# Optimization experiments

Hardware: AMD Instinct MI355X
Metric: run time of the kernel (lower is better)

## Reference

```python
import jax, jax.numpy as jnp
import numpy as np
import math

B, N, D, H, FFN = 64, 128, 128, 4, 128
NEG = -9e15
LRELU_SLOPE = 0.2  # LeakyReLU alpha from init_kwargs


def entmax_bisect(x, alpha, n_iter=30):
    # alpha-entmax via bisection (entmax package algorithm); alpha broadcastable, in (1, 2].
    am1 = alpha - 1.0
    x = x * am1
    d = x.shape[-1]
    max_val = jnp.max(x, axis=-1, keepdims=True)
    tau_lo = max_val - 1.0
    tau_hi = max_val - (1.0 / d) ** am1

    def p(tau):
        return jnp.maximum(x - tau, 0.0) ** (1.0 / am1)

    f_lo = jnp.sum(p(tau_lo), axis=-1, keepdims=True) - 1.0
    for _ in range(n_iter):  # fixed iteration count -> jit friendly
        tau_m = 0.5 * (tau_lo + tau_hi)
        f_m = jnp.sum(p(tau_m), axis=-1, keepdims=True) - 1.0
        same = (f_m * f_lo) >= 0
        tau_lo = jnp.where(same, tau_m, tau_lo)
        f_lo = jnp.where(same, f_m, f_lo)
        tau_hi = jnp.where(same, tau_hi, tau_m)
    pm = p(0.5 * (tau_lo + tau_hi))
    return pm / jnp.sum(pm, axis=-1, keepdims=True)


def layernorm(x, g, b, eps=1e-5):
    mu = jnp.mean(x, axis=-1, keepdims=True)
    var = jnp.var(x, axis=-1, keepdims=True)
    return (x - mu) / jnp.sqrt(var + eps) * g + b


def setup_inputs() -> dict:
    key = jax.random.key(0)
    ks = jax.random.split(key, 24)
    s = 0.05
    sw = 1.0 / math.sqrt(D)
    return {
        "hidden": jax.random.normal(ks[0], (B, N, D), jnp.float32),
        "adj": jax.random.randint(ks[1], (B, N, N), 0, 5, jnp.int32),
        "a0": jax.random.normal(ks[2], (D,), jnp.float32) * s,
        "a1": jax.random.normal(ks[3], (D,), jnp.float32) * s,
        "a2": jax.random.normal(ks[4], (D,), jnp.float32) * s,
        "a3": jax.random.normal(ks[5], (D,), jnp.float32) * s,
        "wa": jax.random.normal(ks[6], (D, 1), jnp.float32) * s,
        "ba": jnp.zeros((1,), jnp.float32),
        "wq": jax.random.normal(ks[7], (D, D), jnp.float32) * sw,
        "bq": jnp.zeros((D,), jnp.float32),
        "wk": jax.random.normal(ks[8], (D, D), jnp.float32) * sw,
        "bk": jnp.zeros((D,), jnp.float32),
        "wv": jax.random.normal(ks[9], (D, D), jnp.float32) * sw,
        "bv": jnp.zeros((D,), jnp.float32),
        "w1": jax.random.normal(ks[10], (D, FFN), jnp.float32) * sw,
        "b1": jnp.zeros((FFN,), jnp.float32),
        "w2": jax.random.normal(ks[11], (FFN, D), jnp.float32) * sw,
        "b2": jnp.zeros((D,), jnp.float32),
        "ln_g": jnp.ones((D,), jnp.float32),
        "ln_b": jnp.zeros((D,), jnp.float32),
        "seq_mask": jnp.ones((B, N), jnp.int32),
        "num_heads": H,
    }


def reference(hidden, adj, a0, a1, a2, a3, wa, ba, wq, bq, wk, bk, wv, bv,
              w1, b1, w2, b2, ln_g, ln_b, seq_mask, num_heads):
    Bs, Ns, Ds = hidden.shape
    hd = Ds // num_heads
    # ---- LocalAggregator: relation-typed graph attention (4 edge types) ----
    # e_r[b,i,j] = leakyrelu(sum_d h[b,i,d]*h[b,j,d]*a_r[d]); same math as the
    # original B x N x N x dim repeat/view/matmul, expressed as one contraction.
    A = jnp.stack([a0, a1, a2, a3], axis=1)  # [D, 4]
    e = jax.nn.leaky_relu(jnp.einsum('bid,bjd,dr->bijr', hidden, hidden, A),
                          LRELU_SLOPE)  # [B, N, N, 4]
    att = jnp.full((Bs, Ns, Ns), NEG, dtype=hidden.dtype)
    for r in range(4):  # adj value r+1 selects relation r (original torch.where order)
        att = jnp.where(adj == r + 1, e[..., r], att)
    att = jax.nn.softmax(att, axis=-1)
    local = jnp.einsum('bij,bjd->bid', att, hidden)  # [B, N, D]
    # ---- get_alpha(flag=3): per-session entmax alpha from last position ----
    a_ent = jax.nn.sigmoid(local[:, -1] @ wa + ba) + 1.0  # [B, 1]
    a_ent = jnp.where(a_ent == 1.0, 1.00001, a_ent)
    a_ent = a_ent[:, :, None, None]  # [B,1,1,1] broadcasts over heads/rows/cols
    # ---- EncoderLayer with entmax-bisect multi-head attention (sparse=True) ----
    q = (local @ wq + bq).reshape(Bs, Ns, num_heads, hd).transpose(0, 2, 1, 3)
    k = (local @ wk + bk).reshape(Bs, Ns, num_heads, hd).transpose(0, 2, 1, 3)
    v = (local @ wv + bv).reshape(Bs, Ns, num_heads, hd).transpose(0, 2, 1, 3)
    scores = jnp.einsum('bhid,bhjd->bhij', q, k) / math.sqrt(Ds)  # note: sqrt(dim), as in source
    scores = jnp.where(seq_mask[:, None, None, :] == 0, -1e9, scores)
    alpha = entmax_bisect(scores, a_ent)
    y = jnp.einsum('bhij,bhjd->bhid', alpha, v)
    y = y.transpose(0, 2, 1, 3).reshape(Bs, Ns, Ds)  # output_layer NOT applied (as in source)
    x = local + y
    y2 = jax.nn.relu(y @ w1 + b1) @ w2 + b2  # FFN applied to y, not x (as in source)
    x = x + y2
    return layernorm(x, ln_g, ln_b)
```

## Files before the change

### kernel.cpp

```cpp
#include <hip/hip_runtime.h>
#include <math.h>

#define BB 64
#define NN 128
#define DD 128
#define HH 4
#define HD 32
#define FFN_ 128

static constexpr float NEGV  = -9000000000000000.0f;
static constexpr float SLOPE = 0.2f;
static constexpr float SCALE = 0.08838834764831845f;
#define NEWTON_ITERS 5

__global__ __launch_bounds__(512) void k_att_local(
    const float* __restrict__ hidden, const int* __restrict__ adj,
    const float* __restrict__ a0, const float* __restrict__ a1,
    const float* __restrict__ a2, const float* __restrict__ a3,
    const float* __restrict__ wa, const float* __restrict__ ba,
    float* __restrict__ local, float* __restrict__ aent_out)
{
    __shared__ __align__(16) float At[4][132];
    __shared__ __align__(16) float hb[128][128];
    __shared__ __align__(16) float att[16][132];

    const int blk = blockIdx.x;
    const int b  = blk >> 3;
    const int i0 = (blk & 7) * 16;
    const int tid = threadIdx.x;

    {
        int r = tid >> 7, d = tid & 127;
        float v = (r == 0) ? a0[d] : (r == 1) ? a1[d] : (r == 2) ? a2[d] : a3[d];
        At[r][d] = v;
    }
    #pragma unroll
    for (int p = 0; p < 8; ++p) {
        int q = tid + 512 * p;
        int r = q >> 5, cq = q & 31;
        *reinterpret_cast<float4*>(&hb[r][4 * (cq ^ (r >> 2))]) =
            *reinterpret_cast<const float4*>(&hidden[(size_t)b * NN * DD + (size_t)r * DD + 4 * cq]);
    }
    __syncthreads();

    {
        const int ig = tid >> 7;
        const int j  = tid & 127;
        const int ib = 4 * ig;
        int a0i = adj[(size_t)b * NN * NN + (size_t)(i0 + ib + 0) * NN + j];
        int a1i = adj[(size_t)b * NN * NN + (size_t)(i0 + ib + 1) * NN + j];
        int a2i = adj[(size_t)b * NN * NN + (size_t)(i0 + ib + 2) * NN + j];
        int a3i = adj[(size_t)b * NN * NN + (size_t)(i0 + ib + 3) * NN + j];
        bool v0 = (a0i >= 1 && a0i <= 4), v1 = (a1i >= 1 && a1i <= 4);
        bool v2 = (a2i >= 1 && a2i <= 4), v3 = (a3i >= 1 && a3i <= 4);
        int r0 = v0 ? (a0i - 1) : 0, r1 = v1 ? (a1i - 1) : 0;
        int r2 = v2 ? (a2i - 1) : 0, r3 = v3 ? (a3i - 1) : 0;
        const int jx = j >> 2;
        const int h0x = (i0 + ib + 0) >> 2, h1x = (i0 + ib + 1) >> 2;
        const int h2x = (i0 + ib + 2) >> 2, h3x = (i0 + ib + 3) >> 2;
        float acc0 = 0.0f, acc1 = 0.0f, acc2 = 0.0f, acc3 = 0.0f;
        #pragma unroll 4
        for (int dq = 0; dq < 32; ++dq) {
            float4 jv = *reinterpret_cast<const float4*>(&hb[j][4 * (dq ^ jx)]);
            float4 h0 = *reinterpret_cast<const float4*>(&hb[i0 + ib + 0][4 * (dq ^ h0x)]);
            float4 h1 = *reinterpret_cast<const float4*>(&hb[i0 + ib + 1][4 * (dq ^ h1x)]);
            float4 h2 = *reinterpret_cast<const float4*>(&hb[i0 + ib + 2][4 * (dq ^ h2x)]);
            float4 h3 = *reinterpret_cast<const float4*>(&hb[i0 + ib + 3][4 * (dq ^ h3x)]);
            float4 A0 = *reinterpret_cast<const float4*>(&At[r0][4 * dq]);
            float4 A1 = *reinterpret_cast<const float4*>(&At[r1][4 * dq]);
            float4 A2 = *reinterpret_cast<const float4*>(&At[r2][4 * dq]);
            float4 A3 = *reinterpret_cast<const float4*>(&At[r3][4 * dq]);
            acc0 += (h0.x * jv.x) * A0.x + (h0.y * jv.y) * A0.y + (h0.z * jv.z) * A0.z + (h0.w * jv.w) * A0.w;
            acc1 += (h1.x * jv.x) * A1.x + (h1.y * jv.y) * A1.y + (h1.z * jv.z) * A1.z + (h1.w * jv.w) * A1.w;
            acc2 += (h2.x * jv.x) * A2.x + (h2.y * jv.y) * A2.y + (h2.z * jv.z) * A2.z + (h2.w * jv.w) * A2.w;
            acc3 += (h3.x * jv.x) * A3.x + (h3.y * jv.y) * A3.y + (h3.z * jv.z) * A3.z + (h3.w * jv.w) * A3.w;
        }
        float e0 = (acc0 > 0.0f) ? acc0 : SLOPE * acc0;
        float e1 = (acc1 > 0.0f) ? acc1 : SLOPE * acc1;
        float e2 = (acc2 > 0.0f) ? acc2 : SLOPE * acc2;
        float e3 = (acc3 > 0.0f) ? acc3 : SLOPE * acc3;
        att[ib + 0][j] = v0 ? e0 : NEGV;
        att[ib + 1][j] = v1 ? e1 : NEGV;
        att[ib + 2][j] = v2 ? e2 : NEGV;
        att[ib + 3][j] = v3 ? e3 : NEGV;
    }
    __syncthreads();

    const int ti = tid >> 5;
    const int tl = tid & 31;

    {
        float x0 = att[ti][tl], x1 = att[ti][tl + 32], x2 = att[ti][tl + 64], x3 = att[ti][tl + 96];
        float m = fmaxf(fmaxf(x0, x1), fmaxf(x2, x3));
        #pragma unroll
        for (int off = 16; off >= 1; off >>= 1) m = fmaxf(m, __shfl_xor(m, off));
        float q0 = __expf(x0 - m), q1 = __expf(x1 - m), q2 = __expf(x2 - m), q3 = __expf(x3 - m);
        float s = (q0 + q1) + (q2 + q3);
        #pragma unroll
        for (int off = 16; off >= 1; off >>= 1) s += __shfl_xor(s, off);
        float invs = 1.0f / s;
        att[ti][tl]      = q0 * invs;
        att[ti][tl + 32] = q1 * invs;
        att[ti][tl + 64] = q2 * invs;
        att[ti][tl + 96] = q3 * invs;
    }

    const int jg = 4 * tl;
    float4 acc4 = make_float4(0.0f, 0.0f, 0.0f, 0.0f);
    #pragma unroll 4
    for (int jq = 0; jq < 32; ++jq) {
        int xc = 4 * (tl ^ jq);
        #pragma unroll
        for (int k = 0; k < 4; ++k) {
            int j = 4 * jq + k;
            float av = att[ti][j];
            float4 h4 = *reinterpret_cast<const float4*>(&hb[j][xc]);
            acc4.x += av * h4.x; acc4.y += av * h4.y;
            acc4.z += av * h4.z; acc4.w += av * h4.w;
        }
    }
    *reinterpret_cast<float4*>(&local[(size_t)b * NN * DD + (size_t)(i0 + ti) * DD + jg]) = acc4;

    if (((blk & 7) == 7) && ti == 15) {
        float4 wa4 = *reinterpret_cast<const float4*>(&wa[jg]);
        float dp = acc4.x * wa4.x + acc4.y * wa4.y + acc4.z * wa4.z + acc4.w * wa4.w;
        #pragma unroll
        for (int off = 16; off >= 1; off >>= 1) dp += __shfl_xor(dp, off, 32);
        if (tl == 0) {
            float z = dp + ba[0];
            float sig = 1.0f / (1.0f + __expf(-z));
            float a = sig + 1.0f;
            if (a == 1.0f) a = 1.00001f;
            aent_out[b] = a;
        }
    }
}

__global__ __launch_bounds__(1024) void k_qkv_entmax(
    const float* __restrict__ local,
    const float* __restrict__ wq, const float* __restrict__ bq,
    const float* __restrict__ wk, const float* __restrict__ bk,
    const float* __restrict__ wv, const float* __restrict__ bv,
    const float* __restrict__ aent, const int* __restrict__ seq_mask,
    float* __restrict__ y)
{
    __shared__ __align__(16) float lb[128][132];
    __shared__ __align__(16) float wQs[128][36];
    __shared__ __align__(16) float wKs[128][36];
    __shared__ __align__(16) float wVs[128][36];
    __shared__ __align__(16) float kx[32][132];
    __shared__ __align__(16) float vL[128][32];
    __shared__ int maskL[NN];
    __shared__ float aent_sh;

    const int blk = blockIdx.x;
    const int b = blk >> 2, h = blk & 3;
    const int tid = threadIdx.x;

    #pragma unroll
    for (int p = 0; p < 4; ++p) {
        int idx = tid + 1024 * p;
        int r = idx >> 5, cq = idx & 31;
        *reinterpret_cast<float4*>(&lb[r][4 * cq]) =
            *reinterpret_cast<const float4*>(&local[(size_t)b * NN * DD + (size_t)r * DD + 4 * cq]);
    }
    {
        int d = tid >> 3, c4 = 4 * (tid & 7);
        size_t off = (size_t)d * DD + h * HD + c4;
        *reinterpret_cast<float4*>(&wQs[d][c4]) = *reinterpret_cast<const float4*>(&wq[off]);
        *reinterpret_cast<float4*>(&wKs[d][c4]) = *reinterpret_cast<const float4*>(&wk[off]);
        *reinterpret_cast<float4*>(&wVs[d][c4]) = *reinterpret_cast<const float4*>(&wv[off]);
    }
    if (tid < NN) maskL[tid] = seq_mask[b * NN + tid];
    if (tid == 0) aent_sh = aent[b];
    __syncthreads();

    const int ty = tid >> 3;
    const int tx = tid & 7;
    const int cg = 4 * tx;

    float4 qac = *reinterpret_cast<const float4*>(&bq[h * HD + cg]);
    float4 kac = *reinterpret_cast<const float4*>(&bk[h * HD + cg]);
    float4 vac = *reinterpret_cast<const float4*>(&bv[h * HD + cg]);
    #pragma unroll 4
    for (int kq = 0; kq < 32; ++kq) {
        float4 a = *reinterpret_cast<const float4*>(&lb[ty][4 * kq]);
        float4 w0 = *reinterpret_cast<const float4*>(&wQs[4 * kq + 0][cg]);
        float4 w1 = *reinterpret_cast<const float4*>(&wQs[4 * kq + 1][cg]);
        float4 w2 = *reinterpret_cast<const float4*>(&wQs[4 * kq + 2][cg]);
        float4 w3 = *reinterpret_cast<const float4*>(&wQs[4 * kq + 3][cg]);
        qac.x += a.x * w0.x + a.y * w1.x + a.z * w2.x + a.w * w3.x;
        qac.y += a.x * w0.y + a.y * w1.y + a.z * w2.y + a.w * w3.y;
        qac.z += a.x * w0.z + a.y * w1.z + a.z * w2.z + a.w * w3.z;
        qac.w += a.x * w0.w + a.y * w1.w + a.z * w2.w + a.w * w3.w;
        w0 = *reinterpret_cast<const float4*>(&wKs[4 * kq + 0][cg]);
        w1 = *reinterpret_cast<const float4*>(&wKs[4 * kq + 1][cg]);
        w2 = *reinterpret_cast<const float4*>(&wKs[4 * kq + 2][cg]);
        w3 = *reinterpret_cast<const float4*>(&wKs[4 * kq + 3][cg]);
        kac.x += a.x * w0.x + a.y * w1.x + a.z * w2.x + a.w * w3.x;
        kac.y += a.x * w0.y + a.y * w1.y + a.z * w2.y + a.w * w3.y;
        kac.z += a.x * w0.z + a.y * w1.z + a.z * w2.z + a.w * w3.z;
        kac.w += a.x * w0.w + a.y * w1.w + a.z * w2.w + a.w * w3.w;
        w0 = *reinterpret_cast<const float4*>(&wVs[4 * kq + 0][cg]);
        w1 = *reinterpret_cast<const float4*>(&wVs[4 * kq + 1][cg]);
        w2 = *reinterpret_cast<const float4*>(&wVs[4 * kq + 2][cg]);
        w3 = *reinterpret_cast<const float4*>(&wVs[4 * kq + 3][cg]);
        vac.x += a.x * w0.x + a.y * w1.x + a.z * w2.x + a.w * w3.x;
        vac.y += a.x * w0.y + a.y * w1.y + a.z * w2.y + a.w * w3.y;
        vac.z += a.x * w0.z + a.y * w1.z + a.z * w2.z + a.w * w3.z;
        vac.w += a.x * w0.w + a.y * w1.w + a.z * w2.w + a.w * w3.w;
    }
    kx[cg + 0][ty] = kac.x;
    kx[cg + 1][ty] = kac.y;
    kx[cg + 2][ty] = kac.z;
    kx[cg + 3][ty] = kac.w;
    *reinterpret_cast<float4*>(&vL[ty][cg]) = vac;
    __syncthreads();

    const int i   = ty;
    const int sub = tx;
    const int c0  = cg;

    const float am1 = aent_sh - 1.0f;
    const float inv = 1.0f / am1;
    const float invm1 = inv - 1.0f;
    const float thi_off = exp2f(-7.0f * am1);
    const float sc = SCALE * am1;
    const float xneg = -1000000000.0f * am1;

    float xv[16];
    #pragma unroll
    for (int s = 0; s < 16; ++s) xv[s] = 0.0f;
    #pragma unroll
    for (int dq = 0; dq < 8; ++dq) {
        float qx = __shfl(qac.x, dq, 8);
        float qy = __shfl(qac.y, dq, 8);
        float qz = __shfl(qac.z, dq, 8);
        float qw = __shfl(qac.w, dq, 8);
        #pragma unroll
        for (int kk = 0; kk < 4; ++kk) {
            int dh = 4 * dq + kk;
            float qv = (kk == 0) ? qx : (kk == 1) ? qy : (kk == 2) ? qz : qw;
            #pragma unroll
            for (int qq = 0; qq < 4; ++qq) {
                float4 k4 = *reinterpret_cast<const float4*>(&kx[dh][c0 + 32 * qq]);
                xv[4 * qq + 0] += qv * k4.x;
                xv[4 * qq + 1] += qv * k4.y;
                xv[4 * qq + 2] += qv * k4.z;
                xv[4 * qq + 3] += qv * k4.w;
            }
        }
    }
    #pragma unroll
    for (int qq = 0; qq < 4; ++qq) {
        int4 m4 = *reinterpret_cast<const int4*>(&maskL[c0 + 32 * qq]);
        xv[4 * qq + 0] = (m4.x == 0) ? xneg : xv[4 * qq + 0] * sc;
        xv[4 * qq + 1] = (m4.y == 0) ? xneg : xv[4 * qq + 1] * sc;
        xv[4 * qq + 2] = (m4.z == 0) ? xneg : xv[4 * qq + 2] * sc;
        xv[4 * qq + 3] = (m4.w == 0) ? xneg : xv[4 * qq + 3] * sc;
    }

    float mx = xv[0];
    #pragma unroll
    for (int s = 1; s < 16; ++s) mx = fmaxf(mx, xv[s]);
    mx = fmaxf(mx, __shfl_xor(mx, 1));
    mx = fmaxf(mx, __shfl_xor(mx, 2));
    mx = fmaxf(mx, __shfl_xor(mx, 4));

    const float hi = mx - thi_off;
    float tau = mx - 1.0f;

    #pragma unroll
    for (int it = 0; it < NEWTON_ITERS; ++it) {
        float ps = 0.0f, ds = 0.0f;
        #pragma unroll
        for (int s = 0; s < 16; ++s) {
            float t = fmaxf(xv[s] - tau, 0.0f);
            float l = __builtin_amdgcn_logf(t);
            float d = __builtin_amdgcn_exp2f(invm1 * l);
            float p = t * d;
            ps += p; ds += d;
        }
        ps += __shfl_xor(ps, 1); ds += __shfl_xor(ds, 1);
        ps += __shfl_xor(ps, 2); ds += __shfl_xor(ds, 2);
        ps += __shfl_xor(ps, 4); ds += __shfl_xor(ds, 4);
        tau = fminf(tau + (ps - 1.0f) * __builtin_amdgcn_rcpf(inv * ds), hi);
    }

    float pm[16];
    float S = 0.0f;
    #pragma unroll
    for (int s = 0; s < 16; ++s) {
        float t = fmaxf(xv[s] - tau, 0.0f);
        float l = __builtin_amdgcn_logf(t);
        float p = t * __builtin_amdgcn_exp2f(invm1 * l);
        pm[s] = p; S += p;
    }
    S += __shfl_xor(S, 1);
    S += __shfl_xor(S, 2);
    S += __shfl_xor(S, 4);
    float invS = 1.0f / S;

    #pragma unroll
    for (int qq = 0; qq < 4; ++qq) {
        float4 a4 = make_float4(pm[4 * qq + 0] * invS, pm[4 * qq + 1] * invS,
                                pm[4 * qq + 2] * invS, pm[4 * qq + 3] * invS);
        *reinterpret_cast<float4*>(&lb[i][c0 + 32 * qq]) = a4;
    }

    float4 accy = make_float4(0.0f, 0.0f, 0.0f, 0.0f);
    const float* arow = &lb[i][0];
    #pragma unroll 4
    for (int q2 = 0; q2 < 32; ++q2) {
        float4 a4 = *reinterpret_cast<const float4*>(arow + 4 * q2);
        float4 v0 = *reinterpret_cast<const float4*>(&vL[4 * q2 + 0][c0]);
        float4 v1 = *reinterpret_cast<const float4*>(&vL[4 * q2 + 1][c0]);
        float4 v2 = *reinterpret_cast<const float4*>(&vL[4 * q2 + 2][c0]);
        float4 v3 = *reinterpret_cast<const float4*>(&vL[4 * q2 + 3][c0]);
        accy.x += a4.x * v0.x + a4.y * v1.x + a4.z * v2.x + a4.w * v3.x;
        accy.y += a4.x * v0.y + a4.y * v1.y + a4.z * v2.y + a4.w * v3.y;
        accy.z += a4.x * v0.z + a4.y * v1.z + a4.z * v2.z + a4.w * v3.z;
        accy.w += a4.x * v0.w + a4.y * v1.w + a4.z * v2.w + a4.w * v3.w;
    }
    *reinterpret_cast<float4*>(&y[(size_t)b * NN * DD + (size_t)i * DD + h * HD + c0]) = accy;
}

__global__ __launch_bounds__(512) void k_ffn_ln(
    const float* __restrict__ yv, const float* __restrict__ w1,
    const float* __restrict__ b1, const float* __restrict__ w2,
    const float* __restrict__ b2, const float* __restrict__ local,
    const float* __restrict__ g, const float* __restrict__ bb,
    float* __restrict__ out)
{
    __shared__ __align__(16) float Bs[128][128];
    __shared__ __align__(16) float As[32][128];
    __shared__ __align__(16) float Zs[32][128];
    const int mt = blockIdx.x;
    const int b  = mt >> 2;
    const int i0 = (mt & 3) * 32;
    const int tid = threadIdx.x;

    #pragma unroll
    for (int p = 0; p < 8; ++p) {
        int idx = tid + 512 * p;
        int d = idx >> 5, cq = idx & 31;
        *reinterpret_cast<float4*>(&Bs[d][4 * cq]) =
            *reinterpret_cast<const float4*>(&w1[d * FFN_ + 4 * cq]);
    }
    #pragma unroll
    for (int p = 0; p < 2; ++p) {
        int idx = tid + 512 * p;
        int row = idx >> 5, kq = idx & 31;
        *reinterpret_cast<float4*>(&As[row][4 * kq]) =
            *reinterpret_cast<const float4*>(&yv[(size_t)b * NN * DD + (size_t)(i0 + row) * DD + 4 * kq]);
    }
    __syncthreads();

    const int tx = tid & 31, ty = tid >> 5;
    const int c0 = 4 * tx;

    {
        float4 bias = *reinterpret_cast<const float4*>(&b1[c0]);
        float acc[2][4];
        #pragma unroll
        for (int i = 0; i < 2; ++i)
            #pragma unroll
            for (int j = 0; j < 4; ++j) acc[i][j] = 0.0f;
        #pragma unroll 2
        for (int kq = 0; kq < 32; ++kq) {
            float4 b0 = *reinterpret_cast<const float4*>(&Bs[4 * kq + 0][c0]);
            float4 b1v = *reinterpret_cast<const float4*>(&Bs[4 * kq + 1][c0]);
            float4 b2v = *reinterpret_cast<const float4*>(&Bs[4 * kq + 2][c0]);
            float4 b3v = *reinterpret_cast<const float4*>(&Bs[4 * kq + 3][c0]);
            #pragma unroll
            for (int i = 0; i < 2; ++i) {
                float4 a = *reinterpret_cast<const float4*>(&As[2 * ty + i][4 * kq]);
                acc[i][0] += a.x * b0.x + a.y * b1v.x + a.z * b2v.x + a.w * b3v.x;
                acc[i][1] += a.x * b0.y + a.y * b1v.y + a.z * b2v.y + a.w * b3v.y;
                acc[i][2] += a.x * b0.z + a.y * b1v.z + a.z * b2v.z + a.w * b3v.z;
                acc[i][3] += a.x * b0.w + a.y * b1v.w + a.z * b2v.w + a.w * b3v.w;
            }
        }
        #pragma unroll
        for (int i = 0; i < 2; ++i) {
            *reinterpret_cast<float4*>(&Zs[2 * ty + i][c0]) =
                make_float4(fmaxf(acc[i][0] + bias.x, 0.0f), fmaxf(acc[i][1] + bias.y, 0.0f),
                            fmaxf(acc[i][2] + bias.z, 0.0f), fmaxf(acc[i][3] + bias.w, 0.0f));
        }
    }
    __syncthreads();

    #pragma unroll
    for (int p = 0; p < 8; ++p) {
        int idx = tid + 512 * p;
        int d = idx >> 5, cq = idx & 31;
        *reinterpret_cast<float4*>(&Bs[d][4 * cq]) =
            *reinterpret_cast<const float4*>(&w2[d * DD + 4 * cq]);
    }
    __syncthreads();

    float4 bias = *reinterpret_cast<const float4*>(&b2[c0]);
    float4 g4 = *reinterpret_cast<const float4*>(&g[c0]);
    float4 bb4 = *reinterpret_cast<const float4*>(&bb[c0]);
    float acc[2][4];
    #pragma unroll
    for (int i = 0; i < 2; ++i)
        #pragma unroll
        for (int j = 0; j < 4; ++j) acc[i][j] = 0.0f;
    #pragma unroll 2
    for (int kq = 0; kq < 32; ++kq) {
        float4 b0 = *reinterpret_cast<const float4*>(&Bs[4 * kq + 0][c0]);
        float4 b1v = *reinterpret_cast<const float4*>(&Bs[4 * kq + 1][c0]);
        float4 b2v = *reinterpret_cast<const float4*>(&Bs[4 * kq + 2][c0]);
        float4 b3v = *reinterpret_cast<const float4*>(&Bs[4 * kq + 3][c0]);
        #pragma unroll
        for (int i = 0; i < 2; ++i) {
            float4 a = *reinterpret_cast<const float4*>(&Zs[2 * ty + i][4 * kq]);
            acc[i][0] += a.x * b0.x + a.y * b1v.x + a.z * b2v.x + a.w * b3v.x;
            acc[i][1] += a.x * b0.y + a.y * b1v.y + a.z * b2v.y + a.w * b3v.y;
            acc[i][2] += a.x * b0.z + a.y * b1v.z + a.z * b2v.z + a.w * b3v.z;
            acc[i][3] += a.x * b0.w + a.y * b1v.w + a.z * b2v.w + a.w * b3v.w;
        }
    }

    #pragma unroll
    for (int i = 0; i < 2; ++i) {
        size_t base = (size_t)b * NN * DD + (size_t)(i0 + 2 * ty + i) * DD + c0;
        float4 l4 = *reinterpret_cast<const float4*>(&local[base]);
        float4 y4 = *reinterpret_cast<const float4*>(&yv[base]);
        float x0 = acc[i][0] + bias.x + l4.x + y4.x;
        float x1 = acc[i][1] + bias.y + l4.y + y4.y;
        float x2 = acc[i][2] + bias.z + l4.z + y4.z;
        float x3 = acc[i][3] + bias.w + l4.w + y4.w;

        float s = (x0 + x1) + (x2 + x3);
        s += __shfl_xor(s, 1); s += __shfl_xor(s, 2); s += __shfl_xor(s, 4);
        s += __shfl_xor(s, 8); s += __shfl_xor(s, 16);
        float mu = s * (1.0f / 128.0f);
        float d0 = x0 - mu, d1 = x1 - mu, d2 = x2 - mu, d3 = x3 - mu;
        float v = (d0 * d0 + d1 * d1) + (d2 * d2 + d3 * d3);
        v += __shfl_xor(v, 1); v += __shfl_xor(v, 2); v += __shfl_xor(v, 4);
        v += __shfl_xor(v, 8); v += __shfl_xor(v, 16);
        float rstd = rsqrtf(v * (1.0f / 128.0f) + 1e-5f);
        float4 o = make_float4(d0 * rstd * g4.x + bb4.x, d1 * rstd * g4.y + bb4.y,
                               d2 * rstd * g4.z + bb4.z, d3 * rstd * g4.w + bb4.w);
        *reinterpret_cast<float4*>(&out[base]) = o;
    }
}

extern "C" void kernel_launch(void* const* d_in, const int* in_sizes, int n_in,
                              void* d_out, int out_size, void* d_ws, size_t ws_size,
                              hipStream_t stream) {
    const float* hidden = (const float*)d_in[0];
    const int*   adj    = (const int*)d_in[1];
    const float* a0 = (const float*)d_in[2];
    const float* a1 = (const float*)d_in[3];
    const float* a2 = (const float*)d_in[4];
    const float* a3 = (const float*)d_in[5];
    const float* wa = (const float*)d_in[6];
    const float* ba = (const float*)d_in[7];
    const float* wq = (const float*)d_in[8];
    const float* bq = (const float*)d_in[9];
    const float* wk = (const float*)d_in[10];
    const float* bk = (const float*)d_in[11];
    const float* wv = (const float*)d_in[12];
    const float* bv = (const float*)d_in[13];
    const float* w1 = (const float*)d_in[14];
    const float* b1 = (const float*)d_in[15];
    const float* w2 = (const float*)d_in[16];
    const float* b2 = (const float*)d_in[17];
    const float* g  = (const float*)d_in[18];
    const float* bb = (const float*)d_in[19];
    const int* seq_mask = (const int*)d_in[20];

    float* ws   = (float*)d_ws;
    float* local = ws;
    float* yv    = ws + 1048576;
    float* aentw = ws + 2 * 1048576;
    float* out   = (float*)d_out;

    k_att_local<<<dim3(512), dim3(512), 0, stream>>>(hidden, adj, a0, a1, a2, a3,
                                                     wa, ba, local, aentw);
    k_qkv_entmax<<<dim3(256), dim3(1024), 0, stream>>>(local, wq, bq, wk, bk, wv, bv,
                                                       aentw, seq_mask, yv);
    k_ffn_ln<<<dim3(256), dim3(512), 0, stream>>>(yv, w1, b1, w2, b2, local, g, bb, out);
}
```

Baseline: 78.96 us.

## Register-tile QKV projection over four rows with split-K shuffle reduction

Restructures the per-head Q/K/V projection so each thread computes four rows times four columns over an eighth of the reduction dimension, then reduces partial sums across lanes with xor shuffles. This reuses each loaded weight float4 across four rows, cutting shared-memory weight traffic per FMA. The projected Q is staged into the now-free wQs buffer and reloaded from LDS instead of broadcast via shuffles, which costs an extra barrier and many shuffle reductions plus higher register pressure.

```diff
diff --git a/kernel.cpp b/kernel.cpp
--- a/kernel.cpp
+++ b/kernel.cpp
@@ -12,6 +12,10 @@
 static constexpr float SLOPE = 0.2f;
 static constexpr float SCALE = 0.08838834764831845f;
 #define NEWTON_ITERS 5
+
+__device__ __forceinline__ float4 f4fma(float s, float4 w, float4 a) {
+    a.x += s * w.x; a.y += s * w.y; a.z += s * w.z; a.w += s * w.w; return a;
+}
 
 __global__ __launch_bounds__(512) void k_att_local(
     const float* __restrict__ hidden, const int* __restrict__ adj,
@@ -175,51 +179,103 @@
     if (tid == 0) aent_sh = aent[b];
     __syncthreads();
 
-    const int ty = tid >> 3;
-    const int tx = tid & 7;
-    const int cg = 4 * tx;
-
-    float4 qac = *reinterpret_cast<const float4*>(&bq[h * HD + cg]);
-    float4 kac = *reinterpret_cast<const float4*>(&bk[h * HD + cg]);
-    float4 vac = *reinterpret_cast<const float4*>(&bv[h * HD + cg]);
-    #pragma unroll 4
-    for (int kq = 0; kq < 32; ++kq) {
-        float4 a = *reinterpret_cast<const float4*>(&lb[ty][4 * kq]);
-        float4 w0 = *reinterpret_cast<const float4*>(&wQs[4 * kq + 0][cg]);
-        float4 w1 = *reinterpret_cast<const float4*>(&wQs[4 * kq + 1][cg]);
-        float4 w2 = *reinterpret_cast<const float4*>(&wQs[4 * kq + 2][cg]);
-        float4 w3 = *reinterpret_cast<const float4*>(&wQs[4 * kq + 3][cg]);
-        qac.x += a.x * w0.x + a.y * w1.x + a.z * w2.x + a.w * w3.x;
-        qac.y += a.x * w0.y + a.y * w1.y + a.z * w2.y + a.w * w3.y;
-        qac.z += a.x * w0.z + a.y * w1.z + a.z * w2.z + a.w * w3.z;
-        qac.w += a.x * w0.w + a.y * w1.w + a.z * w2.w + a.w * w3.w;
-        w0 = *reinterpret_cast<const float4*>(&wKs[4 * kq + 0][cg]);
-        w1 = *reinterpret_cast<const float4*>(&wKs[4 * kq + 1][cg]);
-        w2 = *reinterpret_cast<const float4*>(&wKs[4 * kq + 2][cg]);
-        w3 = *reinterpret_cast<const float4*>(&wKs[4 * kq + 3][cg]);
-        kac.x += a.x * w0.x + a.y * w1.x + a.z * w2.x + a.w * w3.x;
-        kac.y += a.x * w0.y + a.y * w1.y + a.z * w2.y + a.w * w3.y;
-        kac.z += a.x * w0.z + a.y * w1.z + a.z * w2.z + a.w * w3.z;
-        kac.w += a.x * w0.w + a.y * w1.w + a.z * w2.w + a.w * w3.w;
-        w0 = *reinterpret_cast<const float4*>(&wVs[4 * kq + 0][cg]);
-        w1 = *reinterpret_cast<const float4*>(&wVs[4 * kq + 1][cg]);
-        w2 = *reinterpret_cast<const float4*>(&wVs[4 * kq + 2][cg]);
-        w3 = *reinterpret_cast<const float4*>(&wVs[4 * kq + 3][cg]);
-        vac.x += a.x * w0.x + a.y * w1.x + a.z * w2.x + a.w * w3.x;
-        vac.y += a.x * w0.y + a.y * w1.y + a.z * w2.y + a.w * w3.y;
-        vac.z += a.x * w0.z + a.y * w1.z + a.z * w2.z + a.w * w3.z;
-        vac.w += a.x * w0.w + a.y * w1.w + a.z * w2.w + a.w * w3.w;
-    }
-    kx[cg + 0][ty] = kac.x;
-    kx[cg + 1][ty] = kac.y;
-    kx[cg + 2][ty] = kac.z;
-    kx[cg + 3][ty] = kac.w;
-    *reinterpret_cast<float4*>(&vL[ty][cg]) = vac;
-    __syncthreads();
-
-    const int i   = ty;
-    const int sub = tx;
-    const int c0  = cg;
+    {
+        const int tg  = tid >> 5;
+        const int ks  = (tid >> 3) & 3;
+        const int cq8 = tid & 7;
+        const int cgg = 4 * cq8;
+        const int kbase = 8 * ks;
+
+        float4 qa[4], ka[4], va[4];
+        #pragma unroll
+        for (int r = 0; r < 4; ++r) {
+            qa[r] = make_float4(0.0f, 0.0f, 0.0f, 0.0f);
+            ka[r] = make_float4(0.0f, 0.0f, 0.0f, 0.0f);
+            va[r] = make_float4(0.0f, 0.0f, 0.0f, 0.0f);
+        }
+        #pragma unroll 4
+        for (int s = 0; s < 8; ++s) {
+            const int kq = kbase + s;
+            float4 a[4];
+            #pragma unroll
+            for (int r = 0; r < 4; ++r)
+                a[r] = *reinterpret_cast<const float4*>(&lb[4 * tg + r][4 * kq]);
+            {
+                float4 w0 = *reinterpret_cast<const float4*>(&wQs[4 * kq + 0][cgg]);
+                float4 w1 = *reinterpret_cast<const float4*>(&wQs[4 * kq + 1][cgg]);
+                float4 w2 = *reinterpret_cast<const float4*>(&wQs[4 * kq + 2][cgg]);
+                float4 w3 = *reinterpret_cast<const float4*>(&wQs[4 * kq + 3][cgg]);
+                #pragma unroll
+                for (int r = 0; r < 4; ++r) {
+                    qa[r] = f4fma(a[r].x, w0, qa[r]);
+                    qa[r] = f4fma(a[r].y, w1, qa[r]);
+                    qa[r] = f4fma(a[r].z, w2, qa[r]);
+                    qa[r] = f4fma(a[r].w, w3, qa[r]);
+                }
+            }
+            {
+                float4 w0 = *reinterpret_cast<const float4*>(&wKs[4 * kq + 0][cgg]);
+                float4 w1 = *reinterpret_cast<const float4*>(&wKs[4 * kq + 1][cgg]);
+                float4 w2 = *reinterpret_cast<const float4*>(&wKs[4 * kq + 2][cgg]);
+                float4 w3 = *reinterpret_cast<const float4*>(&wKs[4 * kq + 3][cgg]);
+                #pragma unroll
+                for (int r = 0; r < 4; ++r) {
+                    ka[r] = f4fma(a[r].x, w0, ka[r]);
+                    ka[r] = f4fma(a[r].y, w1, ka[r]);
+                    ka[r] = f4fma(a[r].z, w2, ka[r]);
+                    ka[r] = f4fma(a[r].w, w3, ka[r]);
+                }
+            }
+            {
+                float4 w0 = *reinterpret_cast<const float4*>(&wVs[4 * kq + 0][cgg]);
+                float4 w1 = *reinterpret_cast<const float4*>(&wVs[4 * kq + 1][cgg]);
+                float4 w2 = *reinterpret_cast<const float4*>(&wVs[4 * kq + 2][cgg]);
+                float4 w3 = *reinterpret_cast<const float4*>(&wVs[4 * kq + 3][cgg]);
+                #pragma unroll
+                for (int r = 0; r < 4; ++r) {
+                    va[r] = f4fma(a[r].x, w0, va[r]);
+                    va[r] = f4fma(a[r].y, w1, va[r]);
+                    va[r] = f4fma(a[r].z, w2, va[r]);
+                    va[r] = f4fma(a[r].w, w3, va[r]);
+                }
+            }
+        }
+        #pragma unroll
+        for (int r = 0; r < 4; ++r) {
+            qa[r].x += __shfl_xor(qa[r].x, 8);  qa[r].y += __shfl_xor(qa[r].y, 8);
+            qa[r].z += __shfl_xor(qa[r].z, 8);  qa[r].w += __shfl_xor(qa[r].w, 8);
+            qa[r].x += __shfl_xor(qa[r].x, 16); qa[r].y += __shfl_xor(qa[r].y, 16);
+            qa[r].z += __shfl_xor(qa[r].z, 16); qa[r].w += __shfl_xor(qa[r].w, 16);
+            ka[r].x += __shfl_xor(ka[r].x, 8);  ka[r].y += __shfl_xor(ka[r].y, 8);
+            ka[r].z += __shfl_xor(ka[r].z, 8);  ka[r].w += __shfl_xor(ka[r].w, 8);
+            ka[r].x += __shfl_xor(ka[r].x, 16); ka[r].y += __shfl_xor(ka[r].y, 16);
+            ka[r].z += __shfl_xor(ka[r].z, 16); ka[r].w += __shfl_xor(ka[r].w, 16);
+            va[r].x += __shfl_xor(va[r].x, 8);  va[r].y += __shfl_xor(va[r].y, 8);
+            va[r].z += __shfl_xor(va[r].z, 8);  va[r].w += __shfl_xor(va[r].w, 8);
+            va[r].x += __shfl_xor(va[r].x, 16); va[r].y += __shfl_xor(va[r].y, 16);
+            va[r].z += __shfl_xor(va[r].z, 16); va[r].w += __shfl_xor(va[r].w, 16);
+        }
+        float4 qsel = (ks == 0) ? qa[0] : (ks == 1) ? qa[1] : (ks == 2) ? qa[2] : qa[3];
+        float4 ksel = (ks == 0) ? ka[0] : (ks == 1) ? ka[1] : (ks == 2) ? ka[2] : ka[3];
+        float4 vsel = (ks == 0) ? va[0] : (ks == 1) ? va[1] : (ks == 2) ? va[2] : va[3];
+        float4 qb4 = *reinterpret_cast<const float4*>(&bq[h * HD + cgg]);
+        float4 kb4 = *reinterpret_cast<const float4*>(&bk[h * HD + cgg]);
+        float4 vb4 = *reinterpret_cast<const float4*>(&bv[h * HD + cgg]);
+        const int row = 4 * tg + ks;
+        kx[cgg + 0][row] = ksel.x + kb4.x;
+        kx[cgg + 1][row] = ksel.y + kb4.y;
+        kx[cgg + 2][row] = ksel.z + kb4.z;
+        kx[cgg + 3][row] = ksel.w + kb4.w;
+        *reinterpret_cast<float4*>(&vL[row][cgg]) =
+            make_float4(vsel.x + vb4.x, vsel.y + vb4.y, vsel.z + vb4.z, vsel.w + vb4.w);
+        float4 qout = make_float4(qsel.x + qb4.x, qsel.y + qb4.y, qsel.z + qb4.z, qsel.w + qb4.w);
+        __syncthreads();
+        *reinterpret_cast<float4*>(&wQs[row][cgg]) = qout;
+    }
+    __syncthreads();
+
+    const int i   = tid >> 3;
+    const int c0  = 4 * (tid & 7);
 
     const float am1 = aent_sh - 1.0f;
     const float inv = 1.0f / am1;
@@ -233,14 +289,11 @@
     for (int s = 0; s < 16; ++s) xv[s] = 0.0f;
     #pragma unroll
     for (int dq = 0; dq < 8; ++dq) {
-        float qx = __shfl(qac.x, dq, 8);
-        float qy = __shfl(qac.y, dq, 8);
-        float qz = __shfl(qac.z, dq, 8);
-        float qw = __shfl(qac.w, dq, 8);
+        float4 q4 = *reinterpret_cast<const float4*>(&wQs[i][4 * dq]);
         #pragma unroll
         for (int kk = 0; kk < 4; ++kk) {
             int dh = 4 * dq + kk;
-            float qv = (kk == 0) ? qx : (kk == 1) ? qy : (kk == 2) ? qz : qw;
+            float qv = (kk == 0) ? q4.x : (kk == 1) ? q4.y : (kk == 2) ? q4.z : q4.w;
             #pragma unroll
             for (int qq = 0; qq < 4; ++qq) {
                 float4 k4 = *reinterpret_cast<const float4*>(&kx[dh][c0 + 32 * qq]);
```

New measurement: 87.34 us. 10.6% more time.
